# Kernel optimization log

Hardware: AMD Instinct MI355X
Metric: run time of the kernel (lower is better)

## Reference

```python
import jax, jax.numpy as jnp
import numpy as np

N_NODES = 100000
N_EDGES = 400000
N_GRAPHS = 2048
F_IN = 78
HEADS1 = 10
OUT2 = 128


def _gat_conv(x, src, dst, W, a_src, a_dst, b, heads, out_dim):
    """PyG-style GATConv with self-loops already included in (src, dst)."""
    N = x.shape[0]
    h = (x @ W).reshape(N, heads, out_dim)                       # [N,H,D]
    alpha_src = jnp.einsum('nhd,hd->nh', h, a_src)               # [N,H]
    alpha_dst = jnp.einsum('nhd,hd->nh', h, a_dst)               # [N,H]
    e = jax.nn.leaky_relu(alpha_src[src] + alpha_dst[dst], 0.2)  # [E,H]
    # ragged softmax over incoming edges per destination node
    m = jax.ops.segment_max(e, dst, num_segments=N)
    m = jnp.where(jnp.isfinite(m), m, 0.0)
    ex = jnp.exp(e - jax.lax.stop_gradient(m)[dst])
    denom = jax.ops.segment_sum(ex, dst, num_segments=N)
    alpha = ex / (denom[dst] + 1e-16)                            # [E,H]
    msg = h[src] * alpha[:, :, None]                             # [E,H,D]
    out = jax.ops.segment_sum(msg, dst, num_segments=N)          # [N,H,D]
    return out.reshape(N, heads * out_dim) + b


def setup_inputs() -> dict:
    key = jax.random.key(0)
    ks = jax.random.split(key, 24)
    p = lambda k, shape: (jax.random.normal(k, shape, dtype=jnp.float32) * 0.05)
    x = jax.random.normal(ks[0], (N_NODES, F_IN), dtype=jnp.float32)
    edge_index = jax.random.randint(ks[1], (2, N_EDGES), 0, N_NODES, dtype=jnp.int32)
    # sorted batch assignment guaranteeing every graph is non-empty
    batch = ((jnp.arange(N_NODES, dtype=jnp.int32) * N_GRAPHS) // N_NODES).astype(jnp.int32)
    target = jax.random.normal(ks[2], (N_GRAPHS, 1280), dtype=jnp.float32)
    return {
        'x': x, 'edge_index': edge_index, 'batch': batch, 'target': target,
        'W1': p(ks[3], (F_IN, HEADS1 * F_IN)),
        'a_src1': p(ks[4], (HEADS1, F_IN)),
        'a_dst1': p(ks[5], (HEADS1, F_IN)),
        'b1': jnp.zeros((HEADS1 * F_IN,), jnp.float32),
        'W2': p(ks[6], (HEADS1 * F_IN, OUT2)),
        'a_src2': p(ks[7], (1, OUT2)),
        'a_dst2': p(ks[8], (1, OUT2)),
        'b2': jnp.zeros((OUT2,), jnp.float32),
        'w_gate': p(ks[9], (OUT2, 1)),
        'b_gate': jnp.zeros((1,), jnp.float32),
        'W_xt': p(ks[10], (1280, 256)),
        'b_xt': jnp.zeros((256,), jnp.float32),
        'W_fc1': p(ks[11], (512, 1024)),
        'b_fc1': jnp.zeros((1024,), jnp.float32),
        'W_fc2': p(ks[12], (1024, 256)),
        'b_fc2': jnp.zeros((256,), jnp.float32),
        'W_out': p(ks[13], (256, 1)),
        'b_out': jnp.zeros((1,), jnp.float32),
    }


def reference(x, edge_index, batch, target, W1, a_src1, a_dst1, b1,
              W2, a_src2, a_dst2, b2, w_gate, b_gate, W_xt, b_xt,
              W_fc1, b_fc1, W_fc2, b_fc2, W_out, b_out):
    N = x.shape[0]
    loop = jnp.arange(N, dtype=edge_index.dtype)
    src = jnp.concatenate([edge_index[0], loop])   # add self-loops (PyG default)
    dst = jnp.concatenate([edge_index[1], loop])

    h = jax.nn.elu(_gat_conv(x, src, dst, W1, a_src1, a_dst1, b1, HEADS1, F_IN))
    h = _gat_conv(h, src, dst, W2, a_src2, a_dst2, b2, 1, OUT2)
    h = jax.nn.relu(h)                              # [N,128]

    # WeightedSumAndMax readout
    w = jax.nn.sigmoid(h @ w_gate + b_gate)         # [N,1]
    h_sum = jax.ops.segment_sum(h * w, batch, num_segments=N_GRAPHS)  # [B,128]
    h_max = jax.ops.segment_max(h, batch, num_segments=N_GRAPHS)     # [B,128]
    hg = jnp.concatenate([h_sum, h_max], axis=1)    # [B,256]

    xt = target @ W_xt + b_xt                       # [B,256]
    xc = jnp.concatenate([hg, xt], axis=1)          # [B,512]
    xc = jax.nn.relu(xc @ W_fc1 + b_fc1)
    xc = jax.nn.relu(xc @ W_fc2 + b_fc2)
    return xc @ W_out + b_out                       # [B,1]
```

## Files before the change

### kernel.cpp

```cpp
#include <hip/hip_runtime.h>
#include <cstdint>
#include <cstddef>

#define N_NODESC 100000
#define N_EDGESC 400000
#define N_GRAPHSC 2048
#define F_INC 78
#define HEADS1C 10
#define D1C 78
#define F1C 780
#define OUT2C 128
#define E_TOTC (N_EDGESC + N_NODESC)

typedef unsigned short ushort_t;
typedef __attribute__((ext_vector_type(8))) short short8;
typedef __attribute__((ext_vector_type(4))) float f32x4;
typedef __attribute__((ext_vector_type(4))) unsigned int uint4v;
union U4S8 { uint4v u; short8 s; };

static __device__ __forceinline__ float lrelu(float x){ return x > 0.f ? x : 0.2f*x; }

static __device__ __forceinline__ unsigned short f2bf(float f){
  unsigned int u = __float_as_uint(f);
  unsigned int r = (u + 0x7fffu + ((u >> 16) & 1u)) >> 16;
  return (unsigned short)r;
}
static __device__ __forceinline__ float bf2f(unsigned short h){
  return __uint_as_float(((unsigned int)h) << 16);
}

__global__ void k_deg(const int* __restrict__ ei, int* __restrict__ deg){
  int e = blockIdx.x*256 + threadIdx.x;
  if (e >= E_TOTC) return;
  int dst = (e < N_EDGESC) ? ei[N_EDGESC + e] : (e - N_EDGESC);
  atomicAdd(&deg[dst], 1);
}

__global__ __launch_bounds__(1024) void k_scan1(const int* __restrict__ deg,
                                                int* __restrict__ rowptr,
                                                int* __restrict__ bsum){
  __shared__ int s[1024];
  int t = threadIdx.x, i = blockIdx.x*1024 + t;
  int v = (i < N_NODESC) ? deg[i] : 0;
  s[t] = v; __syncthreads();
  for (int d = 1; d < 1024; d <<= 1){
    int xv = (t >= d) ? s[t-d] : 0;
    __syncthreads();
    s[t] += xv;
    __syncthreads();
  }
  if (i < N_NODESC) rowptr[i+1] = s[t];
  if (t == 1023) bsum[blockIdx.x] = s[t];
}

__global__ void k_scan2(int* __restrict__ bsum, int* __restrict__ rowptr, int nb){
  if (threadIdx.x == 0 && blockIdx.x == 0){
    int run = 0;
    for (int b = 0; b < nb; b++){ int v = bsum[b]; bsum[b] = run; run += v; }
    rowptr[0] = 0;
  }
}

__global__ __launch_bounds__(1024) void k_scan3(int* __restrict__ rowptr,
                                                const int* __restrict__ bsum){
  int i = blockIdx.x*1024 + threadIdx.x;
  if (i < N_NODESC) rowptr[i+1] += bsum[blockIdx.x];
}

__global__ void k_scatter(const int* __restrict__ ei, const int* __restrict__ rowptr,
                          int* __restrict__ cnt, int* __restrict__ esrc){
  int e = blockIdx.x*256 + threadIdx.x;
  if (e >= E_TOTC) return;
  int src, dst;
  if (e < N_EDGESC){ src = ei[e]; dst = ei[N_EDGESC + e]; }
  else { src = dst = e - N_EDGESC; }
  int pos = rowptr[dst] + atomicAdd(&cnt[dst], 1);
  esrc[pos] = src;
}

__global__ void k_wa1(const float* __restrict__ W1, const float* __restrict__ a_src1,
                      const float* __restrict__ a_dst1, float* __restrict__ Wa1){
  int i = blockIdx.x*256 + threadIdx.x;
  if (i >= F_INC*2*HEADS1C) return;
  int d = i / (2*HEADS1C), c = i % (2*HEADS1C);
  const float* a = (c < HEADS1C) ? a_src1 : a_dst1;
  int h = (c < HEADS1C) ? c : c - HEADS1C;
  float s = 0.f;
  for (int j = 0; j < D1C; j++) s += W1[d*F1C + h*D1C + j] * a[h*D1C + j];
  Wa1[d*(2*HEADS1C) + c] = s;
}

__global__ void k_att1(const float* __restrict__ x, const float* __restrict__ Wa1,
                       float* __restrict__ att1){
  int i = blockIdx.x*256 + threadIdx.x;
  if (i >= N_NODESC*2*HEADS1C) return;
  int n = i / (2*HEADS1C), c = i % (2*HEADS1C);
  const float* xr = x + (size_t)n*F_INC;
  float s = 0.f;
  for (int d = 0; d < F_INC; d++) s += xr[d] * Wa1[d*(2*HEADS1C) + c];
  att1[i] = s;
}

__global__ void k_stats1(const float* __restrict__ att1, const int* __restrict__ rowptr,
                         const int* __restrict__ esrc, float* __restrict__ stat1){
  int i = blockIdx.x*256 + threadIdx.x;
  if (i >= N_NODESC*HEADS1C) return;
  int n = i / HEADS1C, h = i % HEADS1C;
  float ad = att1[n*20 + 10 + h];
  int b = rowptr[n], e = rowptr[n+1];
  float m = -1e30f;
  for (int p = b; p < e; p += 4){
    int c = e - p; if (c > 4) c = 4;
    float v[4];
    #pragma unroll
    for (int j = 0; j < 4; j++){ int s = esrc[p + (j < c ? j : 0)]; v[j] = att1[s*20 + h]; }
    #pragma unroll
    for (int j = 0; j < 4; j++) if (j < c) m = fmaxf(m, lrelu(v[j] + ad));
  }
  float den = 0.f;
  for (int p = b; p < e; p += 4){
    int c = e - p; if (c > 4) c = 4;
    float v[4];
    #pragma unroll
    for (int j = 0; j < 4; j++){ int s = esrc[p + (j < c ? j : 0)]; v[j] = att1[s*20 + h]; }
    #pragma unroll
    for (int j = 0; j < 4; j++) if (j < c) den += expf(lrelu(v[j] + ad) - m);
  }
  stat1[n*20 + h] = m;
  stat1[n*20 + 10 + h] = 1.f/(den + 1e-16f);
}

__global__ __launch_bounds__(64) void k_agg1(
    const float* __restrict__ x, const float* __restrict__ att1,
    const float* __restrict__ stat1, const int* __restrict__ rowptr,
    const int* __restrict__ esrc, ushort_t* __restrict__ zc, int base){
  __shared__ float xs[4][F_INC];
  __shared__ float al[4][HEADS1C];
  int n = base + blockIdx.x;
  int l = threadIdx.x;
  int b = rowptr[n], e = rowptr[n+1];
  float acc[13];
  #pragma unroll
  for (int k = 0; k < 13; k++) acc[k] = 0.f;
  int hk[13], dk[13];
  #pragma unroll
  for (int k = 0; k < 13; k++){ int f = l + 64*k; hk[k] = f/78; dk[k] = f%78; }
  float ad = 0.f, mm = 0.f, rd = 0.f;
  if (l < HEADS1C){
    ad = att1[n*20 + 10 + l];
    mm = stat1[n*20 + l];
    rd = stat1[n*20 + 10 + l];
  }
  for (int p = b; p < e; p += 4){
    int c = e - p; if (c > 4) c = 4;
    int ss[4];
    #pragma unroll
    for (int j = 0; j < 4; j++) ss[j] = esrc[p + (j < c ? j : 0)];
    if (l < 39){
      #pragma unroll
      for (int j = 0; j < 4; j++){
        float2 v = *(const float2*)(x + (size_t)ss[j]*F_INC + 2*l);
        xs[j][2*l] = v.x; xs[j][2*l+1] = v.y;
      }
    }
    if (l < HEADS1C){
      #pragma unroll
      for (int j = 0; j < 4; j++){
        float ev = lrelu(att1[ss[j]*20 + l] + ad);
        al[j][l] = (j < c) ? expf(ev - mm) * rd : 0.f;
      }
    }
    __syncthreads();
    #pragma unroll
    for (int k = 0; k < 13; k++){
      int f = l + 64*k;
      if (f < F1C){
        float s = al[0][hk[k]]*xs[0][dk[k]] + al[1][hk[k]]*xs[1][dk[k]]
                + al[2][hk[k]]*xs[2][dk[k]] + al[3][hk[k]]*xs[3][dk[k]];
        acc[k] += s;
      }
    }
    __syncthreads();
  }
  #pragma unroll
  for (int k = 0; k < 13; k++){
    int f = l + 64*k;
    if (f < F1C) zc[(size_t)blockIdx.x*F1C + f] = f2bf(acc[k]);
  }
}

__global__ void k_prepW1(const float* __restrict__ W1, ushort_t* __restrict__ W1t){
  int i = blockIdx.x*256 + threadIdx.x;
  if (i >= HEADS1C*80*96) return;
  int h = i / (80*96), rem = i % (80*96), n = rem / 96, k = rem % 96;
  float v = (n < D1C && k < F_INC) ? W1[(size_t)k*F1C + h*D1C + n] : 0.f;
  W1t[i] = f2bf(v);
}

__global__ void k_prepW2f(const float* __restrict__ W2, ushort_t* __restrict__ W2f){
  int i = blockIdx.x*256 + threadIdx.x;
  if (i >= HEADS1C*128*96) return;
  int h = i / (128*96), rem = i % (128*96), n = rem / 96, k = rem % 96;
  float v = (k < D1C) ? W2[(size_t)(h*D1C + k)*OUT2C + n] : 0.f;
  W2f[i] = f2bf(v);
}

__global__ void k_prepWt(const float* __restrict__ W, ushort_t* __restrict__ Wt,
                         int Kdim, int Ndim, int KB){
  int i = blockIdx.x*256 + threadIdx.x;
  if (i >= Ndim*KB) return;
  int n = i / KB, k = i % KB;
  float v = (k < Kdim) ? W[(size_t)k*Ndim + n] : 0.f;
  Wt[i] = f2bf(v);
}

__global__ void k_cast_bf(const float* __restrict__ in, ushort_t* __restrict__ o, int n){
  int i = blockIdx.x*256 + threadIdx.x;
  if (i < n) o[i] = f2bf(in[i]);
}

template<int BN, int NT, int KB, int KVAL, int ACT, bool HASBIAS>
__global__ __launch_bounds__(256) void mfma_gemm(
    const ushort_t* __restrict__ A, const ushort_t* __restrict__ Bt,
    const float* __restrict__ bias, ushort_t* __restrict__ C,
    int M, int N, int lda, int ldc,
    int zsA, int zsBt, int zsC, int zsBias)
{
  __shared__ unsigned int As[64][20];
  __shared__ unsigned int Bs[BN][20];
  int z = blockIdx.z;
  A += (size_t)z*zsA; Bt += (size_t)z*zsBt; C += (size_t)z*zsC;
  const float* bz = HASBIAS ? (bias + (size_t)z*zsBias) : nullptr;
  int m0 = blockIdx.x*64;
  int n0 = blockIdx.y*BN;
  int t = threadIdx.x;
  int w = t >> 6, lane = t & 63;
  int q = lane >> 4, li = lane & 15;
  f32x4 acc[NT];
  #pragma unroll
  for (int i = 0; i < NT; i++) acc[i] = (f32x4){0.f,0.f,0.f,0.f};

  int am = t >> 2;
  int ak0 = (t & 3)*8;
  int gm = m0 + am;
  bool rv = (gm < M);

  #pragma unroll
  for (int ki = 0; ki < KB/32; ki++){
    const int kt = ki*32;
    int nv;
    if (ki == KB/32 - 1){
      int d = KVAL - ak0; nv = d < 0 ? 0 : (d > 8 ? 8 : d);
    } else nv = 8;
    {
      unsigned u0=0u, u1=0u, u2=0u, u3=0u;
      if (rv && nv > 0){
        const unsigned int* ap = (const unsigned int*)(A + (size_t)gm*lda + kt + ak0);
        u0 = ap[0]; u1 = ap[1]; u2 = ap[2]; u3 = ap[3];
        int ndw = nv >> 1;
        if (ndw < 4) u3 = 0u;
        if (ndw < 3) u2 = 0u;
        if (ndw < 2) u1 = 0u;
      }
      int c0 = (t & 3)*4;
      As[am][c0] = u0; As[am][c0+1] = u1; As[am][c0+2] = u2; As[am][c0+3] = u3;
    }
    for (int g = t; g < BN*4; g += 256){
      int n = g >> 2, c0 = (g & 3)*4;
      const unsigned int* bp = (const unsigned int*)(Bt + (size_t)(n0 + n)*KB + kt + c0*2);
      Bs[n][c0] = bp[0]; Bs[n][c0+1] = bp[1]; Bs[n][c0+2] = bp[2]; Bs[n][c0+3] = bp[3];
    }
    __syncthreads();
    U4S8 a; a.u = *(const uint4v*)&As[w*16 + li][q*4];
    #pragma unroll
    for (int nt = 0; nt < NT; nt++){
      U4S8 b; b.u = *(const uint4v*)&Bs[nt*16 + li][q*4];
      acc[nt] = __builtin_amdgcn_mfma_f32_16x16x32_bf16(a.s, b.s, acc[nt], 0, 0, 0);
    }
    __syncthreads();
  }
  #pragma unroll
  for (int nt = 0; nt < NT; nt++){
    int col = n0 + nt*16 + li;
    if (col >= N) continue;
    float bv = HASBIAS ? bz[col] : 0.f;
    #pragma unroll
    for (int r = 0; r < 4; r++){
      int gmr = m0 + w*16 + q*4 + r;
      if (gmr >= M) continue;
      float v = acc[nt][r] + bv;
      if (ACT == 1) v = fmaxf(v, 0.f);
      else if (ACT == 2) v = (v > 0.f) ? v : expm1f(v);
      C[(size_t)gmr*ldc + col] = f2bf(v);
    }
  }
}

__global__ __launch_bounds__(256, 4) void mfma_fused12(
    const ushort_t* __restrict__ zc, const ushort_t* __restrict__ W1t,
    const float* __restrict__ b1, const ushort_t* __restrict__ W2f,
    ushort_t* __restrict__ h2pre, int M)
{
  __shared__ unsigned int Bs[128][52];
  __shared__ unsigned int Ts[64][52];
  int m0 = blockIdx.x*64;
  int t = threadIdx.x;
  int w = t >> 6, lane = t & 63;
  int q = lane >> 4, li = lane & 15;

  f32x4 acc2[8];
  #pragma unroll
  for (int i = 0; i < 8; i++) acc2[i] = (f32x4){0.f,0.f,0.f,0.f};

  for (int i = t; i < 64*9; i += 256) Ts[i/9][39 + i%9] = 0u;

  int ar = m0 + w*16 + li;
  bool rv = (ar < M);
  const unsigned int* abase = (const unsigned int*)(zc + (size_t)ar*F1C);

  auto lda = [&](int h, uint4v* af){
    af[0] = (uint4v){0u,0u,0u,0u};
    af[1] = (uint4v){0u,0u,0u,0u};
    af[2] = (uint4v){0u,0u,0u,0u};
    if (rv){
      const unsigned int* p = abase + h*39 + q*4;
      af[0][0]=p[0];  af[0][1]=p[1];  af[0][2]=p[2];  af[0][3]=p[3];
      af[1][0]=p[16]; af[1][1]=p[17]; af[1][2]=p[18]; af[1][3]=p[19];
      if (q < 2){
        af[2][0]=p[32]; af[2][1]=p[33]; af[2][2]=p[34]; af[2][3]=p[35];
        if (q == 1) af[2][3] = 0u;
      }
    }
  };

  uint4v acur[3], anxt[3];
  lda(0, acur);

  #pragma unroll 1
  for (int h = 0; h < HEADS1C; h++){
    lda(h+1 < HEADS1C ? h+1 : 0, anxt);

    __syncthreads();
    {
      const unsigned int* bp = (const unsigned int*)(W1t + (size_t)h*80*96);
      #pragma unroll
      for (int g0 = 0; g0 < 4; g0++){
        int g = t + g0*256;
        if (g < 960){
          int n = g/12, c0 = (g%12)*4;
          const unsigned int* p = bp + n*48 + c0;
          Bs[n][c0] = p[0]; Bs[n][c0+1] = p[1]; Bs[n][c0+2] = p[2]; Bs[n][c0+3] = p[3];
        }
      }
    }
    float bv[5];
    #pragma unroll
    for (int nt = 0; nt < 5; nt++){
      int col = nt*16 + li;
      bv[nt] = (col < D1C) ? b1[h*D1C + col] : 0.f;
    }
    __syncthreads();

    f32x4 acc1[5];
    #pragma unroll
    for (int i = 0; i < 5; i++) acc1[i] = (f32x4){0.f,0.f,0.f,0.f};
    #pragma unroll
    for (int ki = 0; ki < 3; ki++){
      U4S8 a; a.u = acur[ki];
      #pragma unroll
      for (int nt = 0; nt < 5; nt++){
        U4S8 b; b.u = *(const uint4v*)&Bs[nt*16 + li][ki*16 + q*4];
        acc1[nt] = __builtin_amdgcn_mfma_f32_16x16x32_bf16(a.s, b.s, acc1[nt], 0, 0, 0);
      }
    }
    #pragma unroll
    for (int nt = 0; nt < 5; nt++){
      int col = nt*16 + li;
      #pragma unroll
      for (int r = 0; r < 4; r++){
        int row = w*16 + q*4 + r;
        float v = acc1[nt][r] + bv[nt];
        v = (v > 0.f) ? v : expm1f(v);
        ((ushort_t*)&Ts[row][0])[col] = f2bf(v);
      }
    }
    __syncthreads();

    {
      const unsigned int* bp = (const unsigned int*)(W2f + (size_t)h*128*96);
      #pragma unroll
      for (int g0 = 0; g0 < 6; g0++){
        int g = t + g0*256;
        int n = g/12, c0 = (g%12)*4;
        const unsigned int* p = bp + n*48 + c0;
        Bs[n][c0] = p[0]; Bs[n][c0+1] = p[1]; Bs[n][c0+2] = p[2]; Bs[n][c0+3] = p[3];
      }
    }
    __syncthreads();

    #pragma unroll
    for (int ki = 0; ki < 3; ki++){
      U4S8 a; a.u = *(const uint4v*)&Ts[w*16 + li][ki*16 + q*4];
      #pragma unroll
      for (int nt = 0; nt < 8; nt++){
        U4S8 b; b.u = *(const uint4v*)&Bs[nt*16 + li][ki*16 + q*4];
        acc2[nt] = __builtin_amdgcn_mfma_f32_16x16x32_bf16(a.s, b.s, acc2[nt], 0, 0, 0);
      }
    }
    acur[0] = anxt[0]; acur[1] = anxt[1]; acur[2] = anxt[2];
  }

  #pragma unroll
  for (int nt = 0; nt < 8; nt++){
    int col = nt*16 + li;
    #pragma unroll
    for (int r = 0; r < 4; r++){
      int gmr = m0 + w*16 + q*4 + r;
      if (gmr < M) h2pre[(size_t)gmr*OUT2C + col] = f2bf(acc2[nt][r]);
    }
  }
}

__global__ void k_att2(const ushort_t* __restrict__ h2pre,
                       const float* __restrict__ a_src2,
                       const float* __restrict__ a_dst2, float* __restrict__ att2){
  int n = blockIdx.x*4 + (threadIdx.x >> 6);
  int l = threadIdx.x & 63;
  if (n >= N_NODESC) return;
  const ushort_t* r = h2pre + (size_t)n*OUT2C;
  float v0 = bf2f(r[l]), v1 = bf2f(r[64+l]);
  float p0 = v0*a_src2[l] + v1*a_src2[64+l];
  float p1 = v0*a_dst2[l] + v1*a_dst2[64+l];
  #pragma unroll
  for (int off = 32; off; off >>= 1){
    p0 += __shfl_xor(p0, off);
    p1 += __shfl_xor(p1, off);
  }
  if (l == 0){ att2[n*2] = p0; att2[n*2+1] = p1; }
}

__global__ void k_stats2(const float* __restrict__ att2, const int* __restrict__ rowptr,
                         const int* __restrict__ esrc, float* __restrict__ stat2){
  int n = blockIdx.x*256 + threadIdx.x;
  if (n >= N_NODESC) return;
  float ad = att2[n*2+1];
  int b = rowptr[n], e = rowptr[n+1];
  float m = -1e30f;
  for (int p = b; p < e; p += 4){
    int c = e - p; if (c > 4) c = 4;
    float v[4];
    #pragma unroll
    for (int j = 0; j < 4; j++){ int s = esrc[p + (j < c ? j : 0)]; v[j] = att2[s*2]; }
    #pragma unroll
    for (int j = 0; j < 4; j++) if (j < c) m = fmaxf(m, lrelu(v[j] + ad));
  }
  float den = 0.f;
  for (int p = b; p < e; p += 4){
    int c = e - p; if (c > 4) c = 4;
    float v[4];
    #pragma unroll
    for (int j = 0; j < 4; j++){ int s = esrc[p + (j < c ? j : 0)]; v[j] = att2[s*2]; }
    #pragma unroll
    for (int j = 0; j < 4; j++) if (j < c) den += expf(lrelu(v[j] + ad) - m);
  }
  stat2[n*2] = m;
  stat2[n*2+1] = 1.f/(den + 1e-16f);
}

__global__ void k_agg2(const ushort_t* __restrict__ h2pre,
                       const float* __restrict__ att2,
                       const float* __restrict__ stat2, const int* __restrict__ rowptr,
                       const int* __restrict__ esrc, const float* __restrict__ b2,
                       const float* __restrict__ w_gate, const float* __restrict__ b_gate,
                       float* __restrict__ h2, float* __restrict__ wnode){
  int n = blockIdx.x*4 + (threadIdx.x >> 6);
  int l = threadIdx.x & 63;
  if (n >= N_NODESC) return;
  float ad = att2[n*2+1], m = stat2[n*2], rd = stat2[n*2+1];
  int b = rowptr[n], e = rowptr[n+1];
  float a0 = 0.f, a1 = 0.f;
  for (int p = b; p < e; p += 4){
    int c = e - p; if (c > 4) c = 4;
    int ss[4];
    #pragma unroll
    for (int j = 0; j < 4; j++) ss[j] = esrc[p + (j < c ? j : 0)];
    unsigned u[4]; float at[4];
    #pragma unroll
    for (int j = 0; j < 4; j++) u[j] = *(const unsigned*)(h2pre + (size_t)ss[j]*OUT2C + 2*l);
    #pragma unroll
    for (int j = 0; j < 4; j++) at[j] = att2[ss[j]*2];
    #pragma unroll
    for (int j = 0; j < 4; j++){
      if (j < c){
        float alpha = expf(lrelu(at[j] + ad) - m) * rd;
        a0 += alpha * bf2f((ushort_t)(u[j] & 0xffffu));
        a1 += alpha * bf2f((ushort_t)(u[j] >> 16));
      }
    }
  }
  float v0 = fmaxf(a0 + b2[2*l],   0.f);
  float v1 = fmaxf(a1 + b2[2*l+1], 0.f);
  float2 hv; hv.x = v0; hv.y = v1;
  *(float2*)(h2 + (size_t)n*OUT2C + 2*l) = hv;
  float pp = v0*w_gate[2*l] + v1*w_gate[2*l+1];
  #pragma unroll
  for (int off = 32; off; off >>= 1) pp += __shfl_xor(pp, off);
  if (l == 0) wnode[n] = 1.f/(1.f + expf(-(pp + b_gate[0])));
}

__global__ __launch_bounds__(128) void k_readout(const float* __restrict__ h2,
                                                 const float* __restrict__ wnode,
                                                 const int* __restrict__ batch,
                                                 ushort_t* __restrict__ xcb){
  __shared__ int lohi[2];
  int g = blockIdx.x, t = threadIdx.x;
  if (t == 0){
    int lo = 0, hi = N_NODESC;
    while (lo < hi){ int mid = (lo+hi) >> 1; if (batch[mid] < g) lo = mid+1; else hi = mid; }
    lohi[0] = lo;
    int lo2 = lo; hi = N_NODESC;
    while (lo2 < hi){ int mid = (lo2+hi) >> 1; if (batch[mid] < g+1) lo2 = mid+1; else hi = mid; }
    lohi[1] = lo2;
  }
  __syncthreads();
  int lo = lohi[0], hi = lohi[1];
  float sum = 0.f, mx = 0.f;
  for (int n = lo; n < hi; n++){
    float v = h2[(size_t)n*OUT2C + t];
    sum += v * wnode[n];
    mx = fmaxf(mx, v);
  }
  xcb[(size_t)g*512 + t] = f2bf(sum);
  xcb[(size_t)g*512 + 128 + t] = f2bf(mx);
}

__global__ void k_final(const ushort_t* __restrict__ f2b, const float* __restrict__ W_out,
                        const float* __restrict__ b_out, float* __restrict__ out){
  int g = blockIdx.x*4 + (threadIdx.x >> 6);
  int l = threadIdx.x & 63;
  if (g >= N_GRAPHSC) return;
  float s = 0.f;
  #pragma unroll
  for (int k = 0; k < 4; k++) s += bf2f(f2b[(size_t)g*256 + l + 64*k]) * W_out[l + 64*k];
  #pragma unroll
  for (int off = 32; off; off >>= 1) s += __shfl_xor(s, off);
  if (l == 0) out[g] = s + b_out[0];
}

extern "C" void kernel_launch(void* const* d_in, const int* in_sizes, int n_in,
                              void* d_out, int out_size, void* d_ws, size_t ws_size,
                              hipStream_t stream) {
  const float* x      = (const float*)d_in[0];
  const int*   ei     = (const int*)d_in[1];
  const int*   batch  = (const int*)d_in[2];
  const float* target = (const float*)d_in[3];
  const float* W1     = (const float*)d_in[4];
  const float* a_src1 = (const float*)d_in[5];
  const float* a_dst1 = (const float*)d_in[6];
  const float* b1     = (const float*)d_in[7];
  const float* W2     = (const float*)d_in[8];
  const float* a_src2 = (const float*)d_in[9];
  const float* a_dst2 = (const float*)d_in[10];
  const float* b2     = (const float*)d_in[11];
  const float* w_gate = (const float*)d_in[12];
  const float* b_gate = (const float*)d_in[13];
  const float* W_xt   = (const float*)d_in[14];
  const float* b_xt   = (const float*)d_in[15];
  const float* W_fc1  = (const float*)d_in[16];
  const float* b_fc1  = (const float*)d_in[17];
  const float* W_fc2  = (const float*)d_in[18];
  const float* b_fc2  = (const float*)d_in[19];
  const float* W_out  = (const float*)d_in[20];
  const float* b_out  = (const float*)d_in[21];
  float* out = (float*)d_out;

  const size_t MB = (size_t)1 << 20;
  int C;
  if      (ws_size >= 245*MB) C = 1;
  else if (ws_size >= 150*MB) C = 2;
  else                        C = 4;
  const int R = N_NODESC / C;

  char* p = (char*)d_ws;
  auto carve = [&](size_t bytes) -> char* {
    char* r = p; p += (bytes + 255) & ~(size_t)255; return r;
  };
  int*   deg    = (int*)  carve((size_t)N_NODESC*4);
  int*   rowptr = (int*)  carve((size_t)(N_NODESC+1)*4);
  int*   cnt    = (int*)  carve((size_t)N_NODESC*4);
  int*   esrc   = (int*)  carve((size_t)E_TOTC*4);
  int*   bsum   = (int*)  carve(128*4);
  float* Wa1    = (float*)carve((size_t)F_INC*20*4);
  float* att1   = (float*)carve((size_t)N_NODESC*20*4);
  float* stat1  = (float*)carve((size_t)N_NODESC*20*4);
  float* att2   = (float*)carve((size_t)N_NODESC*2*4);
  float* stat2  = (float*)carve((size_t)N_NODESC*2*4);
  float* wnode  = (float*)carve((size_t)N_NODESC*4);
  ushort_t* W1t   = (ushort_t*)carve((size_t)HEADS1C*80*96*2);
  ushort_t* W2f   = (ushort_t*)carve((size_t)HEADS1C*128*96*2);
  ushort_t* Wxtt  = (ushort_t*)carve((size_t)256*1280*2);
  ushort_t* Wfc1t = (ushort_t*)carve((size_t)1024*512*2);
  ushort_t* Wfc2t = (ushort_t*)carve((size_t)256*1024*2);
  ushort_t* tb    = (ushort_t*)carve((size_t)N_GRAPHSC*1280*2);
  ushort_t* h2pre = (ushort_t*)carve((size_t)N_NODESC*OUT2C*2);
  ushort_t* xcb   = (ushort_t*)carve((size_t)N_GRAPHSC*512*2);
  ushort_t* f1b   = (ushort_t*)carve((size_t)N_GRAPHSC*1024*2);
  ushort_t* f2b   = (ushort_t*)carve((size_t)N_GRAPHSC*256*2);
  size_t big_bytes = (size_t)R*F1C*2 + 4096;
  size_t h2_bytes  = (size_t)N_NODESC*OUT2C*4;
  char*  BIG = carve(big_bytes > h2_bytes ? big_bytes : h2_bytes);
  ushort_t* zc  = (ushort_t*)BIG;
  float* h2 = (float*)BIG;

  hipMemsetAsync(deg, 0, (size_t)N_NODESC*4, stream);
  hipMemsetAsync(cnt, 0, (size_t)N_NODESC*4, stream);

  k_deg<<<(E_TOTC+255)/256, 256, 0, stream>>>(ei, deg);
  int nb = (N_NODESC + 1023)/1024;
  k_scan1<<<nb, 1024, 0, stream>>>(deg, rowptr, bsum);
  k_scan2<<<1, 64, 0, stream>>>(bsum, rowptr, nb);
  k_scan3<<<nb, 1024, 0, stream>>>(rowptr, bsum);
  k_scatter<<<(E_TOTC+255)/256, 256, 0, stream>>>(ei, rowptr, cnt, esrc);

  k_prepW1<<<(HEADS1C*80*96+255)/256, 256, 0, stream>>>(W1, W1t);
  k_prepW2f<<<(HEADS1C*128*96+255)/256, 256, 0, stream>>>(W2, W2f);
  k_prepWt<<<(256*1280+255)/256, 256, 0, stream>>>(W_xt, Wxtt, 1280, 256, 1280);
  k_prepWt<<<(1024*512+255)/256, 256, 0, stream>>>(W_fc1, Wfc1t, 512, 1024, 512);
  k_prepWt<<<(256*1024+255)/256, 256, 0, stream>>>(W_fc2, Wfc2t, 1024, 256, 1024);
  k_cast_bf<<<((N_GRAPHSC*1280)+255)/256, 256, 0, stream>>>(target, tb, N_GRAPHSC*1280);

  k_wa1<<<(F_INC*20+255)/256, 256, 0, stream>>>(W1, a_src1, a_dst1, Wa1);
  k_att1<<<(N_NODESC*20+255)/256, 256, 0, stream>>>(x, Wa1, att1);
  k_stats1<<<(N_NODESC*HEADS1C+255)/256, 256, 0, stream>>>(att1, rowptr, esrc, stat1);

  for (int c = 0; c < C; c++){
    int base = c*R;
    k_agg1<<<R, 64, 0, stream>>>(x, att1, stat1, rowptr, esrc, zc, base);
    mfma_fused12<<<(R+63)/64, 256, 0, stream>>>(
        zc, W1t, b1, W2f, h2pre + (size_t)base*OUT2C, R);
  }

  k_att2<<<(N_NODESC+3)/4, 256, 0, stream>>>(h2pre, a_src2, a_dst2, att2);
  k_stats2<<<(N_NODESC+255)/256, 256, 0, stream>>>(att2, rowptr, esrc, stat2);
  k_agg2<<<(N_NODESC+3)/4, 256, 0, stream>>>(h2pre, att2, stat2, rowptr, esrc,
                                             b2, w_gate, b_gate, h2, wnode);

  k_readout<<<N_GRAPHSC, 128, 0, stream>>>(h2, wnode, batch, xcb);
  mfma_gemm<128,8,1280,32,0,true><<<dim3(N_GRAPHSC/64, 256/128, 1), 256, 0, stream>>>(
      tb, Wxtt, b_xt, xcb + 256, N_GRAPHSC, 256, 1280, 512, 0,0,0,0);
  mfma_gemm<128,8,512,32,1,true><<<dim3(N_GRAPHSC/64, 1024/128, 1), 256, 0, stream>>>(
      xcb, Wfc1t, b_fc1, f1b, N_GRAPHSC, 1024, 512, 1024, 0,0,0,0);
  mfma_gemm<128,8,1024,32,1,true><<<dim3(N_GRAPHSC/64, 256/128, 1), 256, 0, stream>>>(
      f1b, Wfc2t, b_fc2, f2b, N_GRAPHSC, 256, 1024, 256, 0,0,0,0);
  k_final<<<(N_GRAPHSC+3)/4, 256, 0, stream>>>(f2b, W_out, b_out, out);
}
```

Measured before the change: 673.2 us.

## Fuse layer-2 attention scores into fused GEMM, load weights directly, double row tile

The fused two-layer MFMA kernel now handles 128 rows per block instead of 64, so each weight fragment is reused across two row groups. Weight fragments are read straight from global memory into registers instead of being staged through shared memory, which removes most of the __syncthreads barriers. The alpha_src/alpha_dst dot products for layer 2 are computed in the epilogue with lane shuffles, so the separate k_att2 kernel and its re-read of h2pre are gone. In exchange there is more register pressure (launch bounds lowered to 2 blocks), fewer blocks, and repeated global or L2 reads of the weights.

```diff
diff --git a/kernel.cpp b/kernel.cpp
--- a/kernel.cpp
+++ b/kernel.cpp
@@ -296,34 +296,44 @@
   }
 }
 
-__global__ __launch_bounds__(256, 4) void mfma_fused12(
+__global__ __launch_bounds__(256, 2) void mfma_fused12(
     const ushort_t* __restrict__ zc, const ushort_t* __restrict__ W1t,
     const float* __restrict__ b1, const ushort_t* __restrict__ W2f,
-    ushort_t* __restrict__ h2pre, int M)
+    ushort_t* __restrict__ h2pre, float* __restrict__ att2,
+    const float* __restrict__ a_src2, const float* __restrict__ a_dst2,
+    int M)
 {
-  __shared__ unsigned int Bs[128][52];
-  __shared__ unsigned int Ts[64][52];
-  int m0 = blockIdx.x*64;
+  __shared__ unsigned int Ts[128][52];
+  int m0 = blockIdx.x*128;
   int t = threadIdx.x;
   int w = t >> 6, lane = t & 63;
   int q = lane >> 4, li = lane & 15;
 
-  f32x4 acc2[8];
-  #pragma unroll
-  for (int i = 0; i < 8; i++) acc2[i] = (f32x4){0.f,0.f,0.f,0.f};
-
-  for (int i = t; i < 64*9; i += 256) Ts[i/9][39 + i%9] = 0u;
-
-  int ar = m0 + w*16 + li;
-  bool rv = (ar < M);
-  const unsigned int* abase = (const unsigned int*)(zc + (size_t)ar*F1C);
-
-  auto lda = [&](int h, uint4v* af){
+  f32x4 acc2[2][8];
+  #pragma unroll
+  for (int mg = 0; mg < 2; mg++)
+    #pragma unroll
+    for (int i = 0; i < 8; i++) acc2[mg][i] = (f32x4){0.f,0.f,0.f,0.f};
+
+  if (q == 0){
+    #pragma unroll
+    for (int mg = 0; mg < 2; mg++)
+      #pragma unroll
+      for (int j = 0; j < 9; j++) Ts[mg*64 + w*16 + li][39 + j] = 0u;
+  }
+
+  int ar0 = m0 + w*16 + li;
+  int ar1 = ar0 + 64;
+  bool rv0 = (ar0 < M), rv1 = (ar1 < M);
+  const unsigned int* ab0 = (const unsigned int*)(zc + (size_t)ar0*F1C);
+  const unsigned int* ab1 = (const unsigned int*)(zc + (size_t)ar1*F1C);
+
+  auto lda = [&](int h, const unsigned int* ab, bool rv, uint4v* af){
     af[0] = (uint4v){0u,0u,0u,0u};
     af[1] = (uint4v){0u,0u,0u,0u};
     af[2] = (uint4v){0u,0u,0u,0u};
     if (rv){
-      const unsigned int* p = abase + h*39 + q*4;
+      const unsigned int* p = ab + h*39 + q*4;
       af[0][0]=p[0];  af[0][1]=p[1];  af[0][2]=p[2];  af[0][3]=p[3];
       af[1][0]=p[16]; af[1][1]=p[17]; af[1][2]=p[18]; af[1][3]=p[19];
       if (q < 2){
@@ -333,110 +343,113 @@
     }
   };
 
-  uint4v acur[3], anxt[3];
-  lda(0, acur);
+  uint4v a0[3], a1[3], n0[3], n1[3];
+  lda(0, ab0, rv0, a0);
+  lda(0, ab1, rv1, a1);
+
+  const unsigned int* w1dw = (const unsigned int*)W1t;
+  const unsigned int* w2dw = (const unsigned int*)W2f;
 
   #pragma unroll 1
   for (int h = 0; h < HEADS1C; h++){
-    lda(h+1 < HEADS1C ? h+1 : 0, anxt);
-
-    __syncthreads();
-    {
-      const unsigned int* bp = (const unsigned int*)(W1t + (size_t)h*80*96);
-      #pragma unroll
-      for (int g0 = 0; g0 < 4; g0++){
-        int g = t + g0*256;
-        if (g < 960){
-          int n = g/12, c0 = (g%12)*4;
-          const unsigned int* p = bp + n*48 + c0;
-          Bs[n][c0] = p[0]; Bs[n][c0+1] = p[1]; Bs[n][c0+2] = p[2]; Bs[n][c0+3] = p[3];
-        }
-      }
-    }
-    float bv[5];
+    const unsigned int* w1b = w1dw + (size_t)h*80*48;
+    f32x4 acc1[2][5];
+    #pragma unroll
+    for (int mg = 0; mg < 2; mg++)
+      #pragma unroll
+      for (int i = 0; i < 5; i++) acc1[mg][i] = (f32x4){0.f,0.f,0.f,0.f};
+    #pragma unroll
+    for (int ki = 0; ki < 3; ki++){
+      uint4v bw[5];
+      #pragma unroll
+      for (int nt = 0; nt < 5; nt++)
+        bw[nt] = *(const uint4v*)(w1b + (nt*16 + li)*48 + ki*16 + q*4);
+      U4S8 av0; av0.u = a0[ki];
+      U4S8 av1; av1.u = a1[ki];
+      #pragma unroll
+      for (int nt = 0; nt < 5; nt++){
+        U4S8 b; b.u = bw[nt];
+        acc1[0][nt] = __builtin_amdgcn_mfma_f32_16x16x32_bf16(av0.s, b.s, acc1[0][nt], 0, 0, 0);
+        acc1[1][nt] = __builtin_amdgcn_mfma_f32_16x16x32_bf16(av1.s, b.s, acc1[1][nt], 0, 0, 0);
+      }
+    }
     #pragma unroll
     for (int nt = 0; nt < 5; nt++){
       int col = nt*16 + li;
-      bv[nt] = (col < D1C) ? b1[h*D1C + col] : 0.f;
-    }
-    __syncthreads();
-
-    f32x4 acc1[5];
-    #pragma unroll
-    for (int i = 0; i < 5; i++) acc1[i] = (f32x4){0.f,0.f,0.f,0.f};
+      float bv = (col < D1C) ? b1[h*D1C + col] : 0.f;
+      #pragma unroll
+      for (int mg = 0; mg < 2; mg++){
+        #pragma unroll
+        for (int r = 0; r < 4; r++){
+          int row = mg*64 + w*16 + q*4 + r;
+          float v = acc1[mg][nt][r] + bv;
+          v = (v > 0.f) ? v : expm1f(v);
+          ((ushort_t*)&Ts[row][0])[col] = f2bf(v);
+        }
+      }
+    }
+
+    int hn = (h+1 < HEADS1C) ? h+1 : 0;
+    lda(hn, ab0, rv0, n0);
+    lda(hn, ab1, rv1, n1);
+
+    const unsigned int* w2b = w2dw + (size_t)h*128*48;
     #pragma unroll
     for (int ki = 0; ki < 3; ki++){
-      U4S8 a; a.u = acur[ki];
-      #pragma unroll
-      for (int nt = 0; nt < 5; nt++){
-        U4S8 b; b.u = *(const uint4v*)&Bs[nt*16 + li][ki*16 + q*4];
-        acc1[nt] = __builtin_amdgcn_mfma_f32_16x16x32_bf16(a.s, b.s, acc1[nt], 0, 0, 0);
-      }
-    }
-    #pragma unroll
-    for (int nt = 0; nt < 5; nt++){
-      int col = nt*16 + li;
-      #pragma unroll
-      for (int r = 0; r < 4; r++){
-        int row = w*16 + q*4 + r;
-        float v = acc1[nt][r] + bv[nt];
-        v = (v > 0.f) ? v : expm1f(v);
-        ((ushort_t*)&Ts[row][0])[col] = f2bf(v);
-      }
-    }
-    __syncthreads();
-
-    {
-      const unsigned int* bp = (const unsigned int*)(W2f + (size_t)h*128*96);
-      #pragma unroll
-      for (int g0 = 0; g0 < 6; g0++){
-        int g = t + g0*256;
-        int n = g/12, c0 = (g%12)*4;
-        const unsigned int* p = bp + n*48 + c0;
-        Bs[n][c0] = p[0]; Bs[n][c0+1] = p[1]; Bs[n][c0+2] = p[2]; Bs[n][c0+3] = p[3];
-      }
-    }
-    __syncthreads();
-
-    #pragma unroll
-    for (int ki = 0; ki < 3; ki++){
-      U4S8 a; a.u = *(const uint4v*)&Ts[w*16 + li][ki*16 + q*4];
+      U4S8 at0; at0.u = *(const uint4v*)&Ts[w*16 + li][ki*16 + q*4];
+      U4S8 at1; at1.u = *(const uint4v*)&Ts[64 + w*16 + li][ki*16 + q*4];
+      uint4v bw[8];
+      #pragma unroll
+      for (int nt = 0; nt < 8; nt++)
+        bw[nt] = *(const uint4v*)(w2b + (nt*16 + li)*48 + ki*16 + q*4);
       #pragma unroll
       for (int nt = 0; nt < 8; nt++){
-        U4S8 b; b.u = *(const uint4v*)&Bs[nt*16 + li][ki*16 + q*4];
-        acc2[nt] = __builtin_amdgcn_mfma_f32_16x16x32_bf16(a.s, b.s, acc2[nt], 0, 0, 0);
-      }
-    }
-    acur[0] = anxt[0]; acur[1] = anxt[1]; acur[2] = anxt[2];
-  }
-
+        U4S8 b; b.u = bw[nt];
+        acc2[0][nt] = __builtin_amdgcn_mfma_f32_16x16x32_bf16(at0.s, b.s, acc2[0][nt], 0, 0, 0);
+        acc2[1][nt] = __builtin_amdgcn_mfma_f32_16x16x32_bf16(at1.s, b.s, acc2[1][nt], 0, 0, 0);
+      }
+    }
+    #pragma unroll
+    for (int ki = 0; ki < 3; ki++){ a0[ki] = n0[ki]; a1[ki] = n1[ki]; }
+  }
+
+  float as2[8], ad2[8];
   #pragma unroll
   for (int nt = 0; nt < 8; nt++){
     int col = nt*16 + li;
+    as2[nt] = a_src2[col];
+    ad2[nt] = a_dst2[col];
+  }
+  #pragma unroll
+  for (int mg = 0; mg < 2; mg++){
     #pragma unroll
     for (int r = 0; r < 4; r++){
-      int gmr = m0 + w*16 + q*4 + r;
-      if (gmr < M) h2pre[(size_t)gmr*OUT2C + col] = f2bf(acc2[nt][r]);
-    }
-  }
-}
-
-__global__ void k_att2(const ushort_t* __restrict__ h2pre,
-                       const float* __restrict__ a_src2,
-                       const float* __restrict__ a_dst2, float* __restrict__ att2){
-  int n = blockIdx.x*4 + (threadIdx.x >> 6);
-  int l = threadIdx.x & 63;
-  if (n >= N_NODESC) return;
-  const ushort_t* r = h2pre + (size_t)n*OUT2C;
-  float v0 = bf2f(r[l]), v1 = bf2f(r[64+l]);
-  float p0 = v0*a_src2[l] + v1*a_src2[64+l];
-  float p1 = v0*a_dst2[l] + v1*a_dst2[64+l];
-  #pragma unroll
-  for (int off = 32; off; off >>= 1){
-    p0 += __shfl_xor(p0, off);
-    p1 += __shfl_xor(p1, off);
-  }
-  if (l == 0){ att2[n*2] = p0; att2[n*2+1] = p1; }
+      int gmr = m0 + mg*64 + w*16 + q*4 + r;
+      float p0 = 0.f, p1 = 0.f;
+      ushort_t hv[8];
+      #pragma unroll
+      for (int nt = 0; nt < 8; nt++){
+        ushort_t hb = f2bf(acc2[mg][nt][r]);
+        float vb = bf2f(hb);
+        p0 += vb*as2[nt]; p1 += vb*ad2[nt];
+        hv[nt] = hb;
+      }
+      #pragma unroll
+      for (int off = 1; off < 16; off <<= 1){
+        p0 += __shfl_xor(p0, off);
+        p1 += __shfl_xor(p1, off);
+      }
+      if (gmr < M){
+        #pragma unroll
+        for (int nt = 0; nt < 8; nt++)
+          h2pre[(size_t)gmr*OUT2C + nt*16 + li] = hv[nt];
+        if (li == 0){
+          att2[(size_t)gmr*2]     = p0;
+          att2[(size_t)gmr*2 + 1] = p1;
+        }
+      }
+    }
+  }
 }
 
 __global__ void k_stats2(const float* __restrict__ att2, const int* __restrict__ rowptr,
@@ -636,11 +649,11 @@
   for (int c = 0; c < C; c++){
     int base = c*R;
     k_agg1<<<R, 64, 0, stream>>>(x, att1, stat1, rowptr, esrc, zc, base);
-    mfma_fused12<<<(R+63)/64, 256, 0, stream>>>(
-        zc, W1t, b1, W2f, h2pre + (size_t)base*OUT2C, R);
-  }
-
-  k_att2<<<(N_NODESC+3)/4, 256, 0, stream>>>(h2pre, a_src2, a_dst2, att2);
+    mfma_fused12<<<(R+127)/128, 256, 0, stream>>>(
+        zc, W1t, b1, W2f, h2pre + (size_t)base*OUT2C, att2 + (size_t)base*2,
+        a_src2, a_dst2, R);
+  }
+
   k_stats2<<<(N_NODESC+255)/256, 256, 0, stream>>>(att2, rowptr, esrc, stat2);
   k_agg2<<<(N_NODESC+3)/4, 256, 0, stream>>>(h2pre, att2, stat2, rowptr, esrc,
                                              b2, w_gate, b_gate, h2, wnode);
```

Result: slower. 800.7 us (+18.9%).
